# Optimization experiments

Hardware: AMD Instinct MI355X
Metric: run time of the kernel (lower is better)

## Reference

```python
import jax, jax.numpy as jnp
import numpy as np

DIM = 512
HEADS = 8
DIM_HEAD = 64
SCALE = DIM_HEAD ** -0.5


def setup_inputs() -> dict:
    key = jax.random.key(0)
    ks = jax.random.split(key, 4)
    b, n = 4, 2048
    x = jax.random.normal(ks[0], (b, n, DIM), dtype=jnp.float32)
    Wq = jax.random.normal(ks[1], (DIM, HEADS * DIM_HEAD), dtype=jnp.float32) * (DIM ** -0.5)
    Wkv = jax.random.normal(ks[2], (DIM, 2 * HEADS * DIM_HEAD), dtype=jnp.float32) * (DIM ** -0.5)
    Wo = jax.random.normal(ks[3], (HEADS * DIM_HEAD, DIM), dtype=jnp.float32) * ((HEADS * DIM_HEAD) ** -0.5)
    bo = jnp.zeros((DIM,), dtype=jnp.float32)
    return {"x": x, "Wq": Wq, "Wkv": Wkv, "Wo": Wo, "bo": bo}


def reference(x, Wq, Wkv, Wo, bo):
    b, n, _ = x.shape
    # context = x (self-attention path, kv_include_self=False)
    q = x @ Wq                      # [b, n, h*d]
    kv = x @ Wkv                    # [b, n, 2*h*d]
    k, v = jnp.split(kv, 2, axis=-1)

    def split_heads(t):
        return t.reshape(b, n, HEADS, DIM_HEAD).transpose(0, 2, 1, 3)  # [b,h,n,d]

    q, k, v = split_heads(q), split_heads(k), split_heads(v)
    dots = jnp.einsum('bhid,bhjd->bhij', q, k) * SCALE  # [b,h,n,n]
    attn = jax.nn.softmax(dots, axis=-1)
    out = jnp.einsum('bhij,bhjd->bhid', attn, v)        # [b,h,n,d]
    out = out.transpose(0, 2, 1, 3).reshape(b, n, HEADS * DIM_HEAD)
    return out @ Wo + bo
```

## Files before the change

### kernel.cpp

```cpp
#include <hip/hip_runtime.h>
#include <hip/hip_bf16.h>

typedef short bf16x8 __attribute__((ext_vector_type(8)));
typedef float fx4    __attribute__((ext_vector_type(4)));
typedef unsigned uint32x2 __attribute__((ext_vector_type(2)));

#if __has_builtin(__builtin_amdgcn_exp2f)
#define EXP2 __builtin_amdgcn_exp2f
#else
#define EXP2 exp2f
#endif

__device__ __forceinline__ unsigned pk2(float a, float b) {
  union { __hip_bfloat162 h; unsigned u; } cv;
  cv.h = __float22bfloat162_rn(float2{a, b});
  return cv.u;
}
__device__ __forceinline__ uint2 pk4(const fx4& v) {
  uint2 r;
  r.x = pk2(v[0], v[1]);
  r.y = pk2(v[2], v[3]);
  return r;
}

__device__ __forceinline__ void gld16(const void* g, void* l) {
  __builtin_amdgcn_global_load_lds(
      (const __attribute__((address_space(1))) unsigned int*)g,
      (__attribute__((address_space(3))) unsigned int*)l, 16, 0, 0);
}

__device__ __forceinline__ void bar_raw() {
  asm volatile("s_barrier" ::: "memory");
}
__device__ __forceinline__ void bar_lgkm() {
  asm volatile("s_waitcnt lgkmcnt(0)\ns_barrier" ::: "memory");
}
__device__ __forceinline__ void bar_lgkm_vm4() {
  asm volatile("s_waitcnt vmcnt(4) lgkmcnt(0)\ns_barrier" ::: "memory");
}
__device__ __forceinline__ void bar_vm_lgkm() {
  asm volatile("s_waitcnt vmcnt(0) lgkmcnt(0)\ns_barrier" ::: "memory");
}
__device__ __forceinline__ void cfence() { asm volatile("" ::: "memory"); }

__global__ __launch_bounds__(256) void prep_kernel(
    const float* __restrict__ x, const float* __restrict__ Wq,
    const float* __restrict__ Wkv, const float* __restrict__ Wo,
    short* __restrict__ xb, short* __restrict__ WallT, short* __restrict__ WoT,
    float qscale) {
  const int bx = blockIdx.x, tid = threadIdx.x;
  if (bx < 4096) {
    int i = bx * 256 + tid;
    const float4 s = *(const float4*)(x + (size_t)i * 4);
    uint2 o; o.x = pk2(s.x, s.y); o.y = pk2(s.z, s.w);
    *(uint2*)(xb + (size_t)i * 4) = o;
    return;
  }
  __shared__ float t[32][33];
  const int idx = bx - 4096;
  const int wb = idx & 63, kt = (idx >> 6) * 32;
  const bool mode0 = wb < 48;
  const int ct = (mode0 ? wb : wb - 48) * 32;
  const int tx = tid & 31, ty = tid >> 5;
  short* outT = mode0 ? WallT : WoT;
#pragma unroll
  for (int s = 0; s < 4; ++s) {
    int k = kt + ty + s * 8;
    int c = ct + tx;
    float v;
    if (mode0) v = (c < 512) ? Wq[(size_t)k * 512 + c] * qscale
                             : Wkv[(size_t)k * 1024 + (c - 512)];
    else       v = Wo[(size_t)k * 512 + c];
    t[ty + s * 8][tx] = v;
  }
  __syncthreads();
#pragma unroll
  for (int s = 0; s < 4; ++s) {
    int c = ct + ty + s * 8;
    int k = kt + tx;
    unsigned u = __float_as_uint(t[tx][ty + s * 8]);
    u = (u + 0x7fffu + ((u >> 16) & 1u)) >> 16;
    outT[(size_t)c * 512 + k] = (short)u;
  }
}

__global__ __launch_bounds__(256) void gemm_qkv(
    const short* __restrict__ A, const short* __restrict__ Bt,
    short* __restrict__ oq, short* __restrict__ ok, short* __restrict__ ovT) {
  __shared__ short As[2 * 128 * 32];
  __shared__ short Bs[2 * 128 * 32];
  const int K = 512;
  const int tid = threadIdx.x;
  const int wave = tid >> 6, lane = tid & 63;
  const int quad = lane >> 4, l15 = lane & 15;
  const int wm = wave >> 1, wn = wave & 1;
  const int blk = blockIdx.x;
  const int xcd = blk & 7, slot = blk >> 3;
  const int m0 = ((slot / 12) * 8 + xcd) * 128;
  const int n0 = (slot % 12) * 128;
  const bool swapped = (n0 < 1024);

  int arow[4], aoff[4];
#pragma unroll
  for (int c = 0; c < 4; ++c) {
    int u = c * 256 + tid;
    int slab = u >> 9, r2 = u & 511;
    arow[c] = r2 >> 2;
    aoff[c] = slab * 32 + (r2 & 3) * 8;
  }

  fx4 acc[4][4];
#pragma unroll
  for (int i = 0; i < 4; ++i)
#pragma unroll
    for (int j = 0; j < 4; ++j) acc[i][j] = fx4{0.f, 0.f, 0.f, 0.f};

  bf16x8 apre[4];
#pragma unroll
  for (int c = 0; c < 4; ++c)
    apre[c] = *(const bf16x8*)(A + (size_t)(m0 + arow[c]) * K + aoff[c]);

  for (int k0 = 0; k0 < K; k0 += 64) {
    bar_raw();
#pragma unroll
    for (int c = 0; c < 4; ++c)
      *(bf16x8*)(As + (size_t)(c * 256 + tid) * 8) = apre[c];
#pragma unroll
    for (int c = 0; c < 4; ++c) {
      int u = c * 256 + tid;
      int slab = u >> 9, r2 = u & 511;
      gld16(Bt + (size_t)(n0 + (r2 >> 2)) * K + k0 + slab * 32 + (r2 & 3) * 8,
            Bs + (size_t)(c * 256 + wave * 64) * 8);
    }
    cfence();
    {
      int kn = (k0 + 64) & 511;
#pragma unroll
      for (int c = 0; c < 4; ++c)
        apre[c] = *(const bf16x8*)(A + (size_t)(m0 + arow[c]) * K + kn + aoff[c]);
    }
    bar_lgkm_vm4();

#pragma unroll
    for (int ks2 = 0; ks2 < 2; ++ks2) {
      bf16x8 af[4], bfr[4];
#pragma unroll
      for (int i = 0; i < 4; ++i)
        af[i] = *(const bf16x8*)(As + ks2 * 4096 + (wm * 64 + i * 16 + l15) * 32 + quad * 8);
#pragma unroll
      for (int i = 0; i < 4; ++i)
        bfr[i] = *(const bf16x8*)(Bs + ks2 * 4096 + (wn * 64 + i * 16 + l15) * 32 + quad * 8);
      if (swapped) {
#pragma unroll
        for (int mi = 0; mi < 4; ++mi)
#pragma unroll
          for (int ni = 0; ni < 4; ++ni)
            acc[mi][ni] = __builtin_amdgcn_mfma_f32_16x16x32_bf16(bfr[ni], af[mi], acc[mi][ni], 0, 0, 0);
      } else {
#pragma unroll
        for (int mi = 0; mi < 4; ++mi)
#pragma unroll
          for (int ni = 0; ni < 4; ++ni)
            acc[mi][ni] = __builtin_amdgcn_mfma_f32_16x16x32_bf16(af[mi], bfr[ni], acc[mi][ni], 0, 0, 0);
      }
    }
  }

  const int rowb = m0 + wm * 64;
  const int colb = n0 + wn * 64;
  const int cls = n0 >> 9;
  if (cls < 2) {
    short* base = (cls == 0) ? oq : ok;
#pragma unroll
    for (int mi = 0; mi < 4; ++mi) {
      int t = rowb + mi * 16 + l15;
      int bb = t >> 11, ii = t & 2047;
#pragma unroll
      for (int ni = 0; ni < 4; ++ni) {
        int f = (colb + ni * 16 + quad * 4) & 511;
        int hh = f >> 6, dd = f & 63;
        *(uint2*)(base + ((size_t)(bb * 8 + hh) * 2048 + ii) * 64 + dd) = pk4(acc[mi][ni]);
      }
    }
  } else {
#pragma unroll
    for (int mi = 0; mi < 4; ++mi) {
      int rbase = rowb + mi * 16 + quad * 4;
      int bb = rbase >> 11;
      int ii = rbase & 2047;
#pragma unroll
      for (int ni = 0; ni < 4; ++ni) {
        int c = (colb + ni * 16 + l15) & 511;
        int hh = c >> 6, dd = c & 63;
        *(uint2*)(ovT + ((size_t)(bb * 8 + hh) * 64 + dd) * 2048 + ii) = pk4(acc[mi][ni]);
      }
    }
  }
}

__global__ __launch_bounds__(256) void gemm_out(
    const short* __restrict__ A, const short* __restrict__ Bt,
    float* __restrict__ of, const float* __restrict__ bias) {
  __shared__ short As[2 * 64 * 32];
  __shared__ short Bs[2 * 128 * 32];
  const int K = 512, N = 512;
  const int tid = threadIdx.x;
  const int wave = tid >> 6, lane = tid & 63;
  const int quad = lane >> 4, l15 = lane & 15;
  const int wm = wave >> 1, wn = wave & 1;
  const int m0 = blockIdx.y * 64, n0 = blockIdx.x * 128;

  int arow[2], aoff[2], brow[4], boff[4];
#pragma unroll
  for (int c = 0; c < 2; ++c) {
    int u = c * 256 + tid;
    int slab = u >> 8, r2 = u & 255;
    arow[c] = r2 >> 2; aoff[c] = slab * 32 + (r2 & 3) * 8;
  }
#pragma unroll
  for (int c = 0; c < 4; ++c) {
    int u = c * 256 + tid;
    int slab = u >> 9, r2 = u & 511;
    brow[c] = r2 >> 2; boff[c] = slab * 32 + (r2 & 3) * 8;
  }

  fx4 acc[2][4];
#pragma unroll
  for (int i = 0; i < 2; ++i)
#pragma unroll
    for (int j = 0; j < 4; ++j) acc[i][j] = fx4{0.f, 0.f, 0.f, 0.f};

  bf16x8 apre[2], bpre[4];
#pragma unroll
  for (int c = 0; c < 2; ++c)
    apre[c] = *(const bf16x8*)(A + (size_t)(m0 + arow[c]) * K + aoff[c]);
#pragma unroll
  for (int c = 0; c < 4; ++c)
    bpre[c] = *(const bf16x8*)(Bt + (size_t)(n0 + brow[c]) * K + boff[c]);

  for (int k0 = 0; k0 < K; k0 += 64) {
    bar_raw();
#pragma unroll
    for (int c = 0; c < 2; ++c)
      *(bf16x8*)(As + (size_t)(c * 256 + tid) * 8) = apre[c];
#pragma unroll
    for (int c = 0; c < 4; ++c)
      *(bf16x8*)(Bs + (size_t)(c * 256 + tid) * 8) = bpre[c];
    {
      int kn = (k0 + 64) & 511;
#pragma unroll
      for (int c = 0; c < 2; ++c)
        apre[c] = *(const bf16x8*)(A + (size_t)(m0 + arow[c]) * K + kn + aoff[c]);
#pragma unroll
      for (int c = 0; c < 4; ++c)
        bpre[c] = *(const bf16x8*)(Bt + (size_t)(n0 + brow[c]) * K + kn + boff[c]);
    }
    bar_lgkm();

#pragma unroll
    for (int ks2 = 0; ks2 < 2; ++ks2) {
      bf16x8 af[2], bfr[4];
#pragma unroll
      for (int i = 0; i < 2; ++i)
        af[i] = *(const bf16x8*)(As + ks2 * 2048 + (wm * 32 + i * 16 + l15) * 32 + quad * 8);
#pragma unroll
      for (int i = 0; i < 4; ++i)
        bfr[i] = *(const bf16x8*)(Bs + ks2 * 4096 + (wn * 64 + i * 16 + l15) * 32 + quad * 8);
#pragma unroll
      for (int mi = 0; mi < 2; ++mi)
#pragma unroll
        for (int ni = 0; ni < 4; ++ni)
          acc[mi][ni] = __builtin_amdgcn_mfma_f32_16x16x32_bf16(af[mi], bfr[ni], acc[mi][ni], 0, 0, 0);
    }
  }

  const int rowb = m0 + wm * 32;
  const int colb = n0 + wn * 64;
#pragma unroll
  for (int mi = 0; mi < 2; ++mi)
#pragma unroll
    for (int ni = 0; ni < 4; ++ni) {
      int cg = colb + ni * 16 + l15;
      float bv = bias[cg];
#pragma unroll
      for (int r = 0; r < 4; ++r) {
        int rg = rowb + mi * 16 + quad * 4 + r;
        of[(size_t)rg * N + cg] = acc[mi][ni][r] + bv;
      }
    }
}

__global__ __launch_bounds__(256, 2) void attn_kernel(
    const short* __restrict__ Q, const short* __restrict__ K,
    const short* __restrict__ Vt, short* __restrict__ O) {
  __shared__ short Ks[2 * 64 * 64];
  __shared__ short Vs[2 * 64 * 64];

  const int tid = threadIdx.x;
  const int wave = tid >> 6, lane = tid & 63;
  const int quad = lane >> 4, l15 = lane & 15;
  const int blk = blockIdx.x;
  const int xcd = blk & 7, slot = blk >> 3;
  const int bh = (slot >> 4) * 8 + xcd;
  const int qt = slot & 15;
  const int b = bh >> 3, h = bh & 7;
  const int i0 = qt * 128 + wave * 32;

  const int idx0 = tid, idx1 = 256 + tid;
  const int row0 = idx0 >> 3, sg0 = (idx0 & 7) ^ (row0 & 7);
  const int row1 = idx1 >> 3, sg1 = (idx1 & 7) ^ (row1 & 7);
  const short* Kb = K + (size_t)bh * 2048 * 64;
  const short* Vb = Vt + (size_t)bh * 64 * 2048;

  bf16x8 qf[2][2];
#pragma unroll
  for (int it = 0; it < 2; ++it)
#pragma unroll
    for (int ks = 0; ks < 2; ++ks)
      qf[it][ks] = *(const bf16x8*)(Q + ((size_t)bh * 2048 + i0 + it * 16 + l15) * 64 + ks * 32 + quad * 8);

  bf16x8 ones;
#pragma unroll
  for (int c = 0; c < 8; ++c) ones[c] = (short)0x3F80;

  fx4 oacc[2][4];
  fx4 acc_l[2] = { fx4{0.f,0.f,0.f,0.f}, fx4{0.f,0.f,0.f,0.f} };
#pragma unroll
  for (int it = 0; it < 2; ++it)
#pragma unroll
    for (int dt = 0; dt < 4; ++dt) oacc[it][dt] = fx4{0.f, 0.f, 0.f, 0.f};

  auto DMA = [&](int jn, int bufsel) {
    const int nb = bufsel * 4096;
    gld16(Kb + (size_t)(jn + row0) * 64 + sg0 * 8, Ks + nb + wave * 512);
    gld16(Kb + (size_t)(jn + row1) * 64 + sg1 * 8, Ks + nb + 2048 + wave * 512);
    gld16(Vb + (size_t)row0 * 2048 + jn + sg0 * 8, Vs + nb + wave * 512);
    gld16(Vb + (size_t)row1 * 2048 + jn + sg1 * 8, Vs + nb + 2048 + wave * 512);
  };

  auto QK = [&](const short* Kc, fx4 (&s)[2][4]) {
#pragma unroll
    for (int it = 0; it < 2; ++it)
#pragma unroll
      for (int jt = 0; jt < 4; ++jt) s[it][jt] = fx4{0.f, 0.f, 0.f, 0.f};
#pragma unroll
    for (int ks = 0; ks < 2; ++ks) {
#pragma unroll
      for (int jt = 0; jt < 4; ++jt) {
        bf16x8 kf = *(const bf16x8*)(Kc + (jt * 16 + l15) * 64 + (((ks * 4 + quad) ^ (l15 & 7)) * 8));
#pragma unroll
        for (int it = 0; it < 2; ++it)
          s[it][jt] = __builtin_amdgcn_mfma_f32_16x16x32_bf16(kf, qf[it][ks], s[it][jt], 0, 0, 0);
      }
    }
  };

  auto VLOAD = [&](const short* Vc, bf16x8 (&vf)[2][4]) {
#pragma unroll
    for (int kj = 0; kj < 2; ++kj)
#pragma unroll
      for (int dt = 0; dt < 4; ++dt)
        vf[kj][dt] = *(const bf16x8*)(Vc + (dt * 16 + l15) * 64 + (((kj * 4 + quad) ^ (l15 & 7)) * 8));
  };

  auto SMPV = [&](fx4 (&s)[2][4], bf16x8 (&vf)[2][4]) {
#pragma unroll
    for (int it = 0; it < 2; ++it) {
      unsigned W[4][2];
#pragma unroll
      for (int jt = 0; jt < 4; ++jt) {
#pragma unroll
        for (int r = 0; r < 4; ++r) s[it][jt][r] = EXP2(s[it][jt][r]);
        W[jt][0] = pk2(s[it][jt][0], s[it][jt][1]);
        W[jt][1] = pk2(s[it][jt][2], s[it][jt][3]);
      }
#pragma unroll
      for (int k = 0; k < 2; ++k) {
        union { unsigned u[4]; bf16x8 v; } pw;
#pragma unroll
        for (int hh = 0; hh < 2; ++hh) {
          uint32x2 a = __builtin_amdgcn_permlane32_swap(W[2 * k][hh], W[2 * k + 1][hh], false, false);
          uint32x2 t = __builtin_amdgcn_permlane16_swap(a[0], a[1], false, false);
          pw.u[hh] = t[0];
          pw.u[2 + hh] = t[1];
        }
        acc_l[it] = __builtin_amdgcn_mfma_f32_16x16x32_bf16(ones, pw.v, acc_l[it], 0, 0, 0);
#pragma unroll
        for (int dt = 0; dt < 4; ++dt)
          oacc[it][dt] = __builtin_amdgcn_mfma_f32_16x16x32_bf16(vf[k][dt], pw.v, oacc[it][dt], 0, 0, 0);
      }
    }
  };

  fx4 sA[2][4], sB[2][4];
  bf16x8 vfA[2][4], vfB[2][4];

  DMA(0, 0);
  bar_vm_lgkm();
  DMA(64, 1);
  QK(Ks, sA);
  VLOAD(Vs, vfA);

  for (int t1 = 1; t1 <= 29; t1 += 2) {
    bar_vm_lgkm();
    DMA((t1 + 1) << 6, 0);
    QK(Ks + 4096, sB);
    VLOAD(Vs + 4096, vfB);
    SMPV(sA, vfA);
    bar_vm_lgkm();
    DMA((t1 + 2) << 6, 1);
    QK(Ks, sA);
    VLOAD(Vs, vfA);
    SMPV(sB, vfB);
  }

  bar_vm_lgkm();
  QK(Ks + 4096, sB);
  VLOAD(Vs + 4096, vfB);
  SMPV(sA, vfA);
  SMPV(sB, vfB);

#pragma unroll
  for (int it = 0; it < 2; ++it) {
    float inv = __builtin_amdgcn_rcpf(acc_l[it][0]);
    size_t rowbase = ((size_t)b * 2048 + i0 + it * 16 + l15) * 512 + h * 64;
#pragma unroll
    for (int dt = 0; dt < 4; ++dt) {
      fx4 o = oacc[it][dt] * inv;
      *(uint2*)(O + rowbase + dt * 16 + quad * 4) = pk4(o);
    }
  }
}

extern "C" void kernel_launch(void* const* d_in, const int* in_sizes, int n_in,
                              void* d_out, int out_size, void* d_ws, size_t ws_size,
                              hipStream_t stream) {
  const float* x   = (const float*)d_in[0];
  const float* Wq  = (const float*)d_in[1];
  const float* Wkv = (const float*)d_in[2];
  const float* Wo  = (const float*)d_in[3];
  const float* bo  = (const float*)d_in[4];
  float* out = (float*)d_out;

  char* p = (char*)d_ws;
  short* xb    = (short*)p; p += (size_t)8192 * 512 * 2;
  short* WallT = (short*)p; p += (size_t)1536 * 512 * 2;
  short* WoT   = (short*)p; p += (size_t)512 * 512 * 2;
  short* qb    = (short*)p; p += (size_t)32 * 2048 * 64 * 2;
  short* kb    = (short*)p; p += (size_t)32 * 2048 * 64 * 2;
  short* vTb   = (short*)p; p += (size_t)32 * 64 * 2048 * 2;
  short* Ob    = (short*)p; p += (size_t)8192 * 512 * 2;

  const float qscale = 0.125f * 1.4426950408889634f;

  prep_kernel<<<5120, 256, 0, stream>>>(x, Wq, Wkv, Wo, xb, WallT, WoT, qscale);
  gemm_qkv<<<768, 256, 0, stream>>>(xb, WallT, qb, kb, vTb);
  attn_kernel<<<512, 256, 0, stream>>>(qb, kb, vTb, Ob);
  gemm_out<<<dim3(4, 128), 256, 0, stream>>>(Ob, WoT, out, bo);
}
```

Before: 156.4 us.

## Halve attention query tile per block to double grid and occupancy

Each attention block now covers 64 query rows (16 per wave) instead of 128, so the grid doubles to 1024 blocks and the launch bound asks for 4 blocks per CU. V fragments are no longer double-buffered in registers; the single buffer is reloaded after each softmax-PV step. This cuts register pressure to raise occupancy, but K/V tiles are now staged once per 64 queries instead of per 128, doubling K/V global and LDS traffic, and the V loads are less overlapped.

```diff
diff --git a/kernel.cpp b/kernel.cpp
--- a/kernel.cpp
+++ b/kernel.cpp
@@ -290,7 +290,7 @@
     }
 }
 
-__global__ __launch_bounds__(256, 2) void attn_kernel(
+__global__ __launch_bounds__(256, 4) void attn_kernel(
     const short* __restrict__ Q, const short* __restrict__ K,
     const short* __restrict__ Vt, short* __restrict__ O) {
   __shared__ short Ks[2 * 64 * 64];
@@ -301,10 +301,10 @@
   const int quad = lane >> 4, l15 = lane & 15;
   const int blk = blockIdx.x;
   const int xcd = blk & 7, slot = blk >> 3;
-  const int bh = (slot >> 4) * 8 + xcd;
-  const int qt = slot & 15;
+  const int bh = (slot >> 5) * 8 + xcd;
+  const int qt = slot & 31;
   const int b = bh >> 3, h = bh & 7;
-  const int i0 = qt * 128 + wave * 32;
+  const int i0 = qt * 64 + wave * 16;
 
   const int idx0 = tid, idx1 = 256 + tid;
   const int row0 = idx0 >> 3, sg0 = (idx0 & 7) ^ (row0 & 7);
@@ -312,23 +312,19 @@
   const short* Kb = K + (size_t)bh * 2048 * 64;
   const short* Vb = Vt + (size_t)bh * 64 * 2048;
 
-  bf16x8 qf[2][2];
-#pragma unroll
-  for (int it = 0; it < 2; ++it)
-#pragma unroll
-    for (int ks = 0; ks < 2; ++ks)
-      qf[it][ks] = *(const bf16x8*)(Q + ((size_t)bh * 2048 + i0 + it * 16 + l15) * 64 + ks * 32 + quad * 8);
+  bf16x8 qf[2];
+#pragma unroll
+  for (int ks = 0; ks < 2; ++ks)
+    qf[ks] = *(const bf16x8*)(Q + ((size_t)bh * 2048 + i0 + l15) * 64 + ks * 32 + quad * 8);
 
   bf16x8 ones;
 #pragma unroll
   for (int c = 0; c < 8; ++c) ones[c] = (short)0x3F80;
 
-  fx4 oacc[2][4];
-  fx4 acc_l[2] = { fx4{0.f,0.f,0.f,0.f}, fx4{0.f,0.f,0.f,0.f} };
-#pragma unroll
-  for (int it = 0; it < 2; ++it)
-#pragma unroll
-    for (int dt = 0; dt < 4; ++dt) oacc[it][dt] = fx4{0.f, 0.f, 0.f, 0.f};
+  fx4 oacc[4];
+  fx4 acc_l = fx4{0.f, 0.f, 0.f, 0.f};
+#pragma unroll
+  for (int dt = 0; dt < 4; ++dt) oacc[dt] = fx4{0.f, 0.f, 0.f, 0.f};
 
   auto DMA = [&](int jn, int bufsel) {
     const int nb = bufsel * 4096;
@@ -338,19 +334,15 @@
     gld16(Vb + (size_t)row1 * 2048 + jn + sg1 * 8, Vs + nb + 2048 + wave * 512);
   };
 
-  auto QK = [&](const short* Kc, fx4 (&s)[2][4]) {
-#pragma unroll
-    for (int it = 0; it < 2; ++it)
-#pragma unroll
-      for (int jt = 0; jt < 4; ++jt) s[it][jt] = fx4{0.f, 0.f, 0.f, 0.f};
+  auto QK = [&](const short* Kc, fx4 (&s)[4]) {
+#pragma unroll
+    for (int jt = 0; jt < 4; ++jt) s[jt] = fx4{0.f, 0.f, 0.f, 0.f};
 #pragma unroll
     for (int ks = 0; ks < 2; ++ks) {
 #pragma unroll
       for (int jt = 0; jt < 4; ++jt) {
         bf16x8 kf = *(const bf16x8*)(Kc + (jt * 16 + l15) * 64 + (((ks * 4 + quad) ^ (l15 & 7)) * 8));
-#pragma unroll
-        for (int it = 0; it < 2; ++it)
-          s[it][jt] = __builtin_amdgcn_mfma_f32_16x16x32_bf16(kf, qf[it][ks], s[it][jt], 0, 0, 0);
+        s[jt] = __builtin_amdgcn_mfma_f32_16x16x32_bf16(kf, qf[ks], s[jt], 0, 0, 0);
       }
     }
   };
@@ -363,70 +355,66 @@
         vf[kj][dt] = *(const bf16x8*)(Vc + (dt * 16 + l15) * 64 + (((kj * 4 + quad) ^ (l15 & 7)) * 8));
   };
 
-  auto SMPV = [&](fx4 (&s)[2][4], bf16x8 (&vf)[2][4]) {
-#pragma unroll
-    for (int it = 0; it < 2; ++it) {
-      unsigned W[4][2];
-#pragma unroll
-      for (int jt = 0; jt < 4; ++jt) {
-#pragma unroll
-        for (int r = 0; r < 4; ++r) s[it][jt][r] = EXP2(s[it][jt][r]);
-        W[jt][0] = pk2(s[it][jt][0], s[it][jt][1]);
-        W[jt][1] = pk2(s[it][jt][2], s[it][jt][3]);
-      }
-#pragma unroll
-      for (int k = 0; k < 2; ++k) {
-        union { unsigned u[4]; bf16x8 v; } pw;
-#pragma unroll
-        for (int hh = 0; hh < 2; ++hh) {
-          uint32x2 a = __builtin_amdgcn_permlane32_swap(W[2 * k][hh], W[2 * k + 1][hh], false, false);
-          uint32x2 t = __builtin_amdgcn_permlane16_swap(a[0], a[1], false, false);
-          pw.u[hh] = t[0];
-          pw.u[2 + hh] = t[1];
-        }
-        acc_l[it] = __builtin_amdgcn_mfma_f32_16x16x32_bf16(ones, pw.v, acc_l[it], 0, 0, 0);
-#pragma unroll
-        for (int dt = 0; dt < 4; ++dt)
-          oacc[it][dt] = __builtin_amdgcn_mfma_f32_16x16x32_bf16(vf[k][dt], pw.v, oacc[it][dt], 0, 0, 0);
-      }
+  auto SMPV = [&](fx4 (&s)[4], bf16x8 (&vf)[2][4]) {
+    unsigned W[4][2];
+#pragma unroll
+    for (int jt = 0; jt < 4; ++jt) {
+#pragma unroll
+      for (int r = 0; r < 4; ++r) s[jt][r] = EXP2(s[jt][r]);
+      W[jt][0] = pk2(s[jt][0], s[jt][1]);
+      W[jt][1] = pk2(s[jt][2], s[jt][3]);
+    }
+#pragma unroll
+    for (int k = 0; k < 2; ++k) {
+      union { unsigned u[4]; bf16x8 v; } pw;
+#pragma unroll
+      for (int hh = 0; hh < 2; ++hh) {
+        uint32x2 a = __builtin_amdgcn_permlane32_swap(W[2 * k][hh], W[2 * k + 1][hh], false, false);
+        uint32x2 t = __builtin_amdgcn_permlane16_swap(a[0], a[1], false, false);
+        pw.u[hh] = t[0];
+        pw.u[2 + hh] = t[1];
+      }
+      acc_l = __builtin_amdgcn_mfma_f32_16x16x32_bf16(ones, pw.v, acc_l, 0, 0, 0);
+#pragma unroll
+      for (int dt = 0; dt < 4; ++dt)
+        oacc[dt] = __builtin_amdgcn_mfma_f32_16x16x32_bf16(vf[k][dt], pw.v, oacc[dt], 0, 0, 0);
     }
   };
 
-  fx4 sA[2][4], sB[2][4];
-  bf16x8 vfA[2][4], vfB[2][4];
+  fx4 sA[4], sB[4];
+  bf16x8 vf[2][4];
 
   DMA(0, 0);
   bar_vm_lgkm();
   DMA(64, 1);
   QK(Ks, sA);
-  VLOAD(Vs, vfA);
+  VLOAD(Vs, vf);
 
   for (int t1 = 1; t1 <= 29; t1 += 2) {
     bar_vm_lgkm();
     DMA((t1 + 1) << 6, 0);
     QK(Ks + 4096, sB);
-    VLOAD(Vs + 4096, vfB);
-    SMPV(sA, vfA);
+    SMPV(sA, vf);
+    VLOAD(Vs + 4096, vf);
     bar_vm_lgkm();
     DMA((t1 + 2) << 6, 1);
     QK(Ks, sA);
-    VLOAD(Vs, vfA);
-    SMPV(sB, vfB);
+    SMPV(sB, vf);
+    VLOAD(Vs, vf);
   }
 
   bar_vm_lgkm();
   QK(Ks + 4096, sB);
-  VLOAD(Vs + 4096, vfB);
-  SMPV(sA, vfA);
-  SMPV(sB, vfB);
-
-#pragma unroll
-  for (int it = 0; it < 2; ++it) {
-    float inv = __builtin_amdgcn_rcpf(acc_l[it][0]);
-    size_t rowbase = ((size_t)b * 2048 + i0 + it * 16 + l15) * 512 + h * 64;
+  SMPV(sA, vf);
+  VLOAD(Vs + 4096, vf);
+  SMPV(sB, vf);
+
+  {
+    float inv = __builtin_amdgcn_rcpf(acc_l[0]);
+    size_t rowbase = ((size_t)b * 2048 + i0 + l15) * 512 + h * 64;
 #pragma unroll
     for (int dt = 0; dt < 4; ++dt) {
-      fx4 o = oacc[it][dt] * inv;
+      fx4 o = oacc[dt] * inv;
       *(uint2*)(O + rowbase + dt * 16 + quad * 4) = pk4(o);
     }
   }
@@ -455,6 +443,6 @@
 
   prep_kernel<<<5120, 256, 0, stream>>>(x, Wq, Wkv, Wo, xb, WallT, WoT, qscale);
   gemm_qkv<<<768, 256, 0, stream>>>(xb, WallT, qb, kb, vTb);
-  attn_kernel<<<512, 256, 0, stream>>>(qb, kb, vTb, Ob);
+  attn_kernel<<<1024, 256, 0, stream>>>(qb, kb, vTb, Ob);
   gemm_out<<<dim3(4, 128), 256, 0, stream>>>(Ob, WoT, out, bo);
 }
```

Measured after the change: 166.7 us. +6.6%, slower.

## Split attention KV range across two wave groups per block and merge

Applied to the files above, without the earlier changes.

Each attention block now runs 8 waves instead of 4. Two groups of four waves each handle half of the key/value sequence with their own double-buffered LDS region. At the end, the second group writes its partial output and row-sum accumulators to shared memory, and the first group adds them, normalises and stores the result. The V fragment registers are collapsed into a single buffer loaded after each softmax·V step, which cuts register pressure so more waves fit per CU. The cost is a reduction through LDS, barriers that now span 8 waves, and a tighter register budget from the raised launch bounds, which could cause spills.

```diff
diff --git a/kernel.cpp b/kernel.cpp
--- a/kernel.cpp
+++ b/kernel.cpp
@@ -290,27 +290,31 @@
     }
 }
 
-__global__ __launch_bounds__(256, 2) void attn_kernel(
+__global__ __launch_bounds__(512, 4) void attn_kernel(
     const short* __restrict__ Q, const short* __restrict__ K,
     const short* __restrict__ Vt, short* __restrict__ O) {
-  __shared__ short Ks[2 * 64 * 64];
-  __shared__ short Vs[2 * 64 * 64];
+  __shared__ short Ls[2][2][8192];
 
   const int tid = threadIdx.x;
   const int wave = tid >> 6, lane = tid & 63;
   const int quad = lane >> 4, l15 = lane & 15;
+  const int strm = wave >> 2, ws = wave & 3;
   const int blk = blockIdx.x;
   const int xcd = blk & 7, slot = blk >> 3;
   const int bh = (slot >> 4) * 8 + xcd;
   const int qt = slot & 15;
   const int b = bh >> 3, h = bh & 7;
-  const int i0 = qt * 128 + wave * 32;
-
-  const int idx0 = tid, idx1 = 256 + tid;
+  const int i0 = qt * 128 + ws * 32;
+  const int jb = strm << 10;
+
+  const int tid2 = tid & 255;
+  const int idx0 = tid2, idx1 = 256 + tid2;
   const int row0 = idx0 >> 3, sg0 = (idx0 & 7) ^ (row0 & 7);
   const int row1 = idx1 >> 3, sg1 = (idx1 & 7) ^ (row1 & 7);
   const short* Kb = K + (size_t)bh * 2048 * 64;
   const short* Vb = Vt + (size_t)bh * 64 * 2048;
+  short* Kreg = &Ls[strm][0][0];
+  short* Vreg = &Ls[strm][1][0];
 
   bf16x8 qf[2][2];
 #pragma unroll
@@ -330,12 +334,13 @@
 #pragma unroll
     for (int dt = 0; dt < 4; ++dt) oacc[it][dt] = fx4{0.f, 0.f, 0.f, 0.f};
 
-  auto DMA = [&](int jn, int bufsel) {
+  auto DMA = [&](int t, int bufsel) {
+    const int jn = jb + (t << 6);
     const int nb = bufsel * 4096;
-    gld16(Kb + (size_t)(jn + row0) * 64 + sg0 * 8, Ks + nb + wave * 512);
-    gld16(Kb + (size_t)(jn + row1) * 64 + sg1 * 8, Ks + nb + 2048 + wave * 512);
-    gld16(Vb + (size_t)row0 * 2048 + jn + sg0 * 8, Vs + nb + wave * 512);
-    gld16(Vb + (size_t)row1 * 2048 + jn + sg1 * 8, Vs + nb + 2048 + wave * 512);
+    gld16(Kb + (size_t)(jn + row0) * 64 + sg0 * 8, Kreg + nb + ws * 512);
+    gld16(Kb + (size_t)(jn + row1) * 64 + sg1 * 8, Kreg + nb + 2048 + ws * 512);
+    gld16(Vb + (size_t)row0 * 2048 + jn + sg0 * 8, Vreg + nb + ws * 512);
+    gld16(Vb + (size_t)row1 * 2048 + jn + sg1 * 8, Vreg + nb + 2048 + ws * 512);
   };
 
   auto QK = [&](const short* Kc, fx4 (&s)[2][4]) {
@@ -393,41 +398,65 @@
   };
 
   fx4 sA[2][4], sB[2][4];
-  bf16x8 vfA[2][4], vfB[2][4];
+  bf16x8 vf[2][4];
 
   DMA(0, 0);
   bar_vm_lgkm();
-  DMA(64, 1);
-  QK(Ks, sA);
-  VLOAD(Vs, vfA);
-
-  for (int t1 = 1; t1 <= 29; t1 += 2) {
+  DMA(1, 1);
+  QK(Kreg, sA);
+  VLOAD(Vreg, vf);
+
+  for (int t1 = 1; t1 <= 13; t1 += 2) {
     bar_vm_lgkm();
-    DMA((t1 + 1) << 6, 0);
-    QK(Ks + 4096, sB);
-    VLOAD(Vs + 4096, vfB);
-    SMPV(sA, vfA);
+    DMA(t1 + 1, 0);
+    QK(Kreg + 4096, sB);
+    SMPV(sA, vf);
+    VLOAD(Vreg + 4096, vf);
     bar_vm_lgkm();
-    DMA((t1 + 2) << 6, 1);
-    QK(Ks, sA);
-    VLOAD(Vs, vfA);
-    SMPV(sB, vfB);
+    DMA(t1 + 2, 1);
+    QK(Kreg, sA);
+    SMPV(sB, vf);
+    VLOAD(Vreg, vf);
   }
 
   bar_vm_lgkm();
-  QK(Ks + 4096, sB);
-  VLOAD(Vs + 4096, vfB);
-  SMPV(sA, vfA);
-  SMPV(sB, vfB);
-
-#pragma unroll
-  for (int it = 0; it < 2; ++it) {
-    float inv = __builtin_amdgcn_rcpf(acc_l[it][0]);
-    size_t rowbase = ((size_t)b * 2048 + i0 + it * 16 + l15) * 512 + h * 64;
-#pragma unroll
-    for (int dt = 0; dt < 4; ++dt) {
-      fx4 o = oacc[it][dt] * inv;
-      *(uint2*)(O + rowbase + dt * 16 + quad * 4) = pk4(o);
+  QK(Kreg + 4096, sB);
+  SMPV(sA, vf);
+  VLOAD(Vreg + 4096, vf);
+  SMPV(sB, vf);
+
+  float* F = (float*)&Ls[0][0][0];
+  bar_lgkm();
+  if (strm == 1) {
+    const int base = (ws * 64 + lane) * 36;
+#pragma unroll
+    for (int it = 0; it < 2; ++it)
+#pragma unroll
+      for (int dt = 0; dt < 4; ++dt)
+        *(fx4*)&F[base + (it * 4 + dt) * 4] = oacc[it][dt];
+    F[base + 32] = acc_l[0][0];
+    F[base + 33] = acc_l[1][0];
+  }
+  bar_lgkm();
+  if (strm == 0) {
+    const int base = (ws * 64 + lane) * 36;
+#pragma unroll
+    for (int it = 0; it < 2; ++it)
+#pragma unroll
+      for (int dt = 0; dt < 4; ++dt)
+        oacc[it][dt] += *(const fx4*)&F[base + (it * 4 + dt) * 4];
+    float lt[2];
+    lt[0] = acc_l[0][0] + F[base + 32];
+    lt[1] = acc_l[1][0] + F[base + 33];
+#pragma unroll
+    for (int it = 0; it < 2; ++it) {
+      float inv = __builtin_amdgcn_rcpf(lt[it]);
+      size_t rowbase = ((size_t)b * 2048 + i0 + it * 16 + l15) * 512 + h * 64;
+#pragma unroll
+      for (int dt = 0; dt < 4; ++dt) {
+        fx4 o = oacc[it][dt] * inv;
+        *(uint2*)(O + rowbase + dt * 16 + quad * 4) = pk4(o);
+      }
     }
   }
 }
@@ -455,6 +484,6 @@
 
   prep_kernel<<<5120, 256, 0, stream>>>(x, Wq, Wkv, Wo, xb, WallT, WoT, qscale);
   gemm_qkv<<<768, 256, 0, stream>>>(xb, WallT, qb, kb, vTb);
-  attn_kernel<<<512, 256, 0, stream>>>(qb, kb, vTb, Ob);
+  attn_kernel<<<512, 512, 0, stream>>>(qb, kb, vTb, Ob);
   gemm_out<<<dim3(4, 128), 256, 0, stream>>>(Ob, WoT, out, bo);
 }
```

Result: slower. 318.1 us (+103.4%).
